# Kernel tuning notes

Hardware: AMD Instinct MI355X
Metric: run time of the kernel (lower is better)

## Reference

```python
import jax, jax.numpy as jnp
import numpy as np

B, T, D, H, O = 64, 2048, 64, 512, 128


def setup_inputs() -> dict:
    key = jax.random.key(0)
    ks = jax.random.split(key, 7)
    s = 1.0 / np.sqrt(H).astype(np.float32)  # PyTorch default uniform(-1/sqrt(H), 1/sqrt(H))
    u = lambda k, shp: jax.random.uniform(k, shp, jnp.float32, -s, s)
    return {
        "x": jax.random.normal(ks[0], (B, T, D), jnp.float32),
        "W_ih": u(ks[1], (4 * H, D)),
        "W_hh": u(ks[2], (4 * H, H)),
        "b_ih": u(ks[3], (4 * H,)),
        "b_hh": u(ks[4], (4 * H,)),
        "W_out": u(ks[5], (O, H)),
        "b_out": u(ks[6], (O,)),
        "batch_size": B,
    }


def reference(x, W_ih, W_hh, b_ih, b_hh, W_out, b_out, batch_size):
    Bv, Tv, Dv = x.shape
    Hv = W_hh.shape[1]
    # Precompute input-to-gate projections for all timesteps: [T, B, 4H]
    xg = (jnp.einsum("btd,gd->btg", x, W_ih) + b_ih + b_hh).transpose(1, 0, 2)
    h0 = jnp.zeros((Bv, Hv), x.dtype)
    c0 = jnp.zeros((Bv, Hv), x.dtype)

    def step(carry, g_t):
        h, c = carry
        g = g_t + h @ W_hh.T  # [B, 4H]
        i, f, gc, o = jnp.split(g, 4, axis=-1)  # PyTorch gate order i,f,g,o
        i = jax.nn.sigmoid(i)
        f = jax.nn.sigmoid(f)
        gc = jnp.tanh(gc)
        o = jax.nn.sigmoid(o)
        c = f * c + i * gc
        h = o * jnp.tanh(c)
        return (h, c), None

    (hT, cT), _ = jax.lax.scan(step, (h0, c0), xg)
    # Linear applied at last timestep only (module returns predictions[:, -1, :])
    pred = hT @ W_out.T + b_out  # [B, O]
    return pred, hT[None], cT[None]  # (pred, h_n[1,B,H], c_n[1,B,H])
```

## Files before the change

kernel.cpp:

```cpp
#include <hip/hip_runtime.h>
#include <hip/hip_bf16.h>


typedef short short8 __attribute__((ext_vector_type(8)));
typedef float floatx4 __attribute__((ext_vector_type(4)));

#define T_STEPS 2048
#define NBG 4
#define NGI 32
#define SB() __builtin_amdgcn_sched_barrier(0)

__device__ __forceinline__ unsigned short f2bf(float f){
    unsigned u = __builtin_bit_cast(unsigned, f);
    u += 0x7FFFu + ((u >> 16) & 1u);
    return (unsigned short)(u >> 16);
}

__device__ __forceinline__ short8 pack8(float4 a, float4 b){
    short8 s;
    s[0]=(short)f2bf(a.x); s[1]=(short)f2bf(a.y); s[2]=(short)f2bf(a.z); s[3]=(short)f2bf(a.w);
    s[4]=(short)f2bf(b.x); s[5]=(short)f2bf(b.y); s[6]=(short)f2bf(b.z); s[7]=(short)f2bf(b.w);
    return s;
}

__device__ __forceinline__ float fsigmoid(float x){ return 1.0f/(1.0f+__expf(-x)); }
__device__ __forceinline__ float ftanh(float x){ return 2.0f*fsigmoid(2.0f*x)-1.0f; }

__device__ __forceinline__ void xload4(float4* X, const float* base){
    asm volatile(
    "global_load_dwordx4 %0, %4, off\n\t"
    "global_load_dwordx4 %1, %4, off offset:16\n\t"
    "global_load_dwordx4 %2, %4, off offset:128\n\t"
    "global_load_dwordx4 %3, %4, off offset:144"
    : "=&v"(X[0]), "=&v"(X[1]), "=&v"(X[2]), "=&v"(X[3])
    : "v"(base) : "memory");
}

__device__ __forceinline__ void hload16_sc1(short8* A, const unsigned short* base){
    asm volatile(
    "global_load_dwordx4 %0, %16, off sc1\n\t"
    "global_load_dwordx4 %1, %16, off offset:64 sc1\n\t"
    "global_load_dwordx4 %2, %16, off offset:128 sc1\n\t"
    "global_load_dwordx4 %3, %16, off offset:192 sc1\n\t"
    "global_load_dwordx4 %4, %16, off offset:256 sc1\n\t"
    "global_load_dwordx4 %5, %16, off offset:320 sc1\n\t"
    "global_load_dwordx4 %6, %16, off offset:384 sc1\n\t"
    "global_load_dwordx4 %7, %16, off offset:448 sc1\n\t"
    "global_load_dwordx4 %8, %16, off offset:512 sc1\n\t"
    "global_load_dwordx4 %9, %16, off offset:576 sc1\n\t"
    "global_load_dwordx4 %10, %16, off offset:640 sc1\n\t"
    "global_load_dwordx4 %11, %16, off offset:704 sc1\n\t"
    "global_load_dwordx4 %12, %16, off offset:768 sc1\n\t"
    "global_load_dwordx4 %13, %16, off offset:832 sc1\n\t"
    "global_load_dwordx4 %14, %16, off offset:896 sc1\n\t"
    "global_load_dwordx4 %15, %16, off offset:960 sc1"
    : "=&v"(A[0]), "=&v"(A[1]), "=&v"(A[2]), "=&v"(A[3]),
      "=&v"(A[4]), "=&v"(A[5]), "=&v"(A[6]), "=&v"(A[7]),
      "=&v"(A[8]), "=&v"(A[9]), "=&v"(A[10]), "=&v"(A[11]),
      "=&v"(A[12]), "=&v"(A[13]), "=&v"(A[14]), "=&v"(A[15])
    : "v"(base) : "memory");
}

__global__ __launch_bounds__(64, 1)
void lstm_persist(const float* __restrict__ x,
                  const float* __restrict__ W_ih,
                  const float* __restrict__ W_hh,
                  const float* __restrict__ b_ih,
                  const float* __restrict__ b_hh,
                  const float* __restrict__ W_out,
                  const float* __restrict__ b_out,
                  float* __restrict__ out,
                  unsigned short* __restrict__ hbuf,
                  unsigned* __restrict__ flags)
{
    const int wg   = blockIdx.x;
    const int bg   = wg & 3;
    const int gi   = wg >> 2;
    const int lane = threadIdx.x;
    const int ln   = lane & 15;
    const int lk   = lane >> 4;
    const int hd0  = gi << 4;

    __shared__ __align__(16) unsigned short hl[256];

    short8 bw[4][18];
#pragma unroll
    for (int g = 0; g < 4; ++g){
        const int row = g * 512 + hd0 + ln;
        const float* pih = W_ih + row * 64 + lk * 8;
#pragma unroll
        for (int kk = 0; kk < 2; ++kk){
            float4 u0 = *reinterpret_cast<const float4*>(pih + kk * 32);
            float4 u1 = *reinterpret_cast<const float4*>(pih + kk * 32 + 4);
            bw[g][kk] = pack8(u0, u1);
        }
        const float* phh = W_hh + row * 512 + lk * 8;
#pragma unroll
        for (int kk = 2; kk < 18; ++kk){
            float4 u0 = *reinterpret_cast<const float4*>(phh + (kk - 2) * 32);
            float4 u1 = *reinterpret_cast<const float4*>(phh + (kk - 2) * 32 + 4);
            bw[g][kk] = pack8(u0, u1);
        }
    }

    float bias[4];
#pragma unroll
    for (int g = 0; g < 4; ++g){
        const int col = g * 512 + hd0 + ln;
        bias[g] = b_ih[col] + b_hh[col];
    }

    float c0 = 0.f, c1 = 0.f, c2 = 0.f, c3 = 0.f;
    const int xrow = bg * 16 + ln;

    const unsigned* fpoll = flags + bg * NGI + (lane & 31);
    unsigned* fme = flags + bg * NGI + gi;
    const unsigned one = 1u;

    short8 a[18];
    short8 stv = {0,0,0,0,0,0,0,0};
    float4 xr[4];
    xload4(xr, x + ((size_t)xrow * T_STEPS) * 64 + lk * 8);

    for (int t = 0; t < T_STEPS; ++t){
        const unsigned short* hp =
            hbuf + (size_t)((((t & 1) ^ 1) * NBG + bg) * 16 + ln) * 512 + lk * 8;

        if (t > 0){
            unsigned fv;
            do {
                asm volatile("global_load_dword %0, %1, off sc1\n\t"
                             "s_waitcnt vmcnt(0)"
                             : "=v"(fv) : "v"(fpoll) : "memory");
            } while (!__all((int)(fv >= (unsigned)t)));
            SB();
            asm volatile("" :: "v"(stv));
            hload16_sc1(&a[2], hp);
        } else {
            asm volatile("s_waitcnt vmcnt(0)" ::: "memory");
            SB();
            asm volatile("" :: "v"(stv));
        }

        a[0] = pack8(xr[0], xr[1]);
        a[1] = pack8(xr[2], xr[3]);

        floatx4 acc0 = {bias[0], bias[0], bias[0], bias[0]};
        floatx4 acc1 = {bias[1], bias[1], bias[1], bias[1]};
        floatx4 acc2 = {bias[2], bias[2], bias[2], bias[2]};
        floatx4 acc3 = {bias[3], bias[3], bias[3], bias[3]};
#pragma unroll
        for (int kk = 0; kk < 2; ++kk){
            acc0 = __builtin_amdgcn_mfma_f32_16x16x32_bf16(a[kk], bw[0][kk], acc0, 0, 0, 0);
            acc1 = __builtin_amdgcn_mfma_f32_16x16x32_bf16(a[kk], bw[1][kk], acc1, 0, 0, 0);
            acc2 = __builtin_amdgcn_mfma_f32_16x16x32_bf16(a[kk], bw[2][kk], acc2, 0, 0, 0);
            acc3 = __builtin_amdgcn_mfma_f32_16x16x32_bf16(a[kk], bw[3][kk], acc3, 0, 0, 0);
        }

        if (t > 0){
            asm volatile("s_waitcnt vmcnt(0)" ::: "memory");
            SB();
            const unsigned expst = (((unsigned)(t - 1) >> 1) & 1u) + 1u;
            for (;;){
                int ok = 1;
#pragma unroll
                for (int c = 2; c < 18; ++c){
                    unsigned s = ((unsigned)(unsigned short)a[c][6] & 1u)
                               | (((unsigned)(unsigned short)a[c][7] & 1u) << 1);
                    ok &= (s == expst) ? 1 : 0;
                }
                if (__all(ok)) break;
                hload16_sc1(&a[2], hp);
                asm volatile("s_waitcnt vmcnt(0)" ::: "memory");
                SB();
            }
#pragma unroll
            for (int kk = 2; kk < 18; ++kk){
                acc0 = __builtin_amdgcn_mfma_f32_16x16x32_bf16(a[kk], bw[0][kk], acc0, 0, 0, 0);
                acc1 = __builtin_amdgcn_mfma_f32_16x16x32_bf16(a[kk], bw[1][kk], acc1, 0, 0, 0);
                acc2 = __builtin_amdgcn_mfma_f32_16x16x32_bf16(a[kk], bw[2][kk], acc2, 0, 0, 0);
                acc3 = __builtin_amdgcn_mfma_f32_16x16x32_bf16(a[kk], bw[3][kk], acc3, 0, 0, 0);
            }
        }

#define EPI(R, CREG)                                                         \
        {   float iv = fsigmoid(acc0[R]);                                    \
            float fv_ = fsigmoid(acc1[R]);                                   \
            float gv = ftanh(acc2[R]);                                       \
            float ov = fsigmoid(acc3[R]);                                    \
            CREG = fv_ * CREG + iv * gv;                                     \
            float hv = ov * ftanh(CREG);                                     \
            hl[(lk * 4 + R) * 16 + ln] = f2bf(hv);                           \
            if (t == T_STEPS - 1){                                           \
                int rr = bg * 16 + lk * 4 + R;                               \
                out[8192  + rr * 512 + hd0 + ln] = hv;                       \
                out[40960 + rr * 512 + hd0 + ln] = CREG;                     \
            }                                                                \
        }
        EPI(0, c0) EPI(1, c1) EPI(2, c2) EPI(3, c3)
#undef EPI

        {
            const int tn = (t + 1 < T_STEPS) ? (t + 1) : t;
            xload4(xr, x + ((size_t)xrow * T_STEPS + (size_t)tn) * 64 + lk * 8);
        }

        asm volatile("s_waitcnt lgkmcnt(0)" ::: "memory");

        {
            const unsigned stamp = (((unsigned)t >> 1) & 1u) + 1u;
            if (lane < 32){
                const int row = lane >> 1, half = lane & 1;
                short8 v = *reinterpret_cast<const short8*>(&hl[row * 16 + half * 8]);
                v[6] = (short)((v[6] & ~(short)1) | (short)(stamp & 1u));
                v[7] = (short)((v[7] & ~(short)1) | (short)((stamp >> 1) & 1u));
                stv = v;
                unsigned short* dst =
                    hbuf + (size_t)(((t & 1) * NBG + bg) * 16 + row) * 512 + hd0 + half * 8;
                asm volatile("global_store_dwordx4 %0, %1, off sc1"
                             :: "v"(dst), "v"(stv) : "memory");
            }
            if (lane == 0){
                asm volatile("global_atomic_add %0, %1, off sc1"
                             :: "v"(fme), "v"(one) : "memory");
            }
        }
    }

    if (gi == 0){
        unsigned fv;
        do {
            asm volatile("global_load_dword %0, %1, off sc1\n\t"
                         "s_waitcnt vmcnt(0)"
                         : "=v"(fv) : "v"(fpoll) : "memory");
        } while (!__all((int)(fv >= (unsigned)T_STEPS)));
        SB();
        const unsigned expst = (((unsigned)(T_STEPS - 1) >> 1) & 1u) + 1u;
        const unsigned short* hp =
            hbuf + (size_t)((1 * NBG + bg) * 16 + ln) * 512 + lk * 8;
        short8 ha[16];
        int ok;
        do {
            hload16_sc1(ha, hp);
            asm volatile("s_waitcnt vmcnt(0)" ::: "memory");
            SB();
            ok = 1;
#pragma unroll
            for (int kk = 0; kk < 16; ++kk){
                unsigned s = ((unsigned)(unsigned short)ha[kk][6] & 1u)
                           | (((unsigned)(unsigned short)ha[kk][7] & 1u) << 1);
                ok &= (s == expst) ? 1 : 0;
            }
        } while (!__all(ok));
        SB();
#pragma unroll
        for (int o0 = 0; o0 < 8; ++o0){
            const int col = o0 * 16 + ln;
            const float* wp = W_out + col * 512 + lk * 8;
            floatx4 pa = {0.f, 0.f, 0.f, 0.f};
#pragma unroll
            for (int kk = 0; kk < 16; ++kk){
                float4 w0 = *reinterpret_cast<const float4*>(wp + kk * 32);
                float4 w1 = *reinterpret_cast<const float4*>(wp + kk * 32 + 4);
                pa = __builtin_amdgcn_mfma_f32_16x16x32_bf16(ha[kk], pack8(w0, w1), pa, 0, 0, 0);
            }
            const float bo = b_out[col];
#pragma unroll
            for (int r = 0; r < 4; ++r){
                const int rr = bg * 16 + lk * 4 + r;
                out[rr * 128 + col] = pa[r] + bo;
            }
        }
    }
}

extern "C" void kernel_launch(void* const* d_in, const int* in_sizes, int n_in,
                              void* d_out, int out_size, void* d_ws, size_t ws_size,
                              hipStream_t stream) {
    const float* x     = (const float*)d_in[0];
    const float* W_ih  = (const float*)d_in[1];
    const float* W_hh  = (const float*)d_in[2];
    const float* b_ih  = (const float*)d_in[3];
    const float* b_hh  = (const float*)d_in[4];
    const float* W_out = (const float*)d_in[5];
    const float* b_out = (const float*)d_in[6];

    const size_t HBUF_BYTES = (size_t)2 * NBG * 16 * 512 * 2;
    unsigned short* hbuf = (unsigned short*)d_ws;
    unsigned* flags = (unsigned*)((char*)d_ws + HBUF_BYTES);

    hipMemsetAsync(hbuf, 0, HBUF_BYTES, stream);
    hipMemsetAsync(flags, 0, NBG * NGI * sizeof(unsigned), stream);
    lstm_persist<<<dim3(NBG * NGI), dim3(64), 0, stream>>>(
        x, W_ih, W_hh, b_ih, b_hh, W_out, b_out,
        (float*)d_out, hbuf, flags);
}
```

Baseline: 6.783 ms.

## Spread workgroups across XCDs and rework cross-block handoff coherence

Launches 256 workgroups and maps them so that batch group is wg&7 with half the groups exiting early. With round-robin XCD dispatch, each batch group's blocks then land on one XCD, which may let a cheaper cache scope serve the exchange. The h-state loads switch from sc1 to sc0 scope, and polling alternates between sc0 and sc1. The store is now followed by a vmcnt wait before the flag atomic, replacing the stamp-bit validation loop at the end. This trades the stamp-based retry scheme for store-then-signal ordering, and relies on the co-location assumption for correctness.

```diff
diff --git a/kernel.cpp b/kernel.cpp
--- a/kernel.cpp
+++ b/kernel.cpp
@@ -33,6 +33,31 @@
     "global_load_dwordx4 %2, %4, off offset:128\n\t"
     "global_load_dwordx4 %3, %4, off offset:144"
     : "=&v"(X[0]), "=&v"(X[1]), "=&v"(X[2]), "=&v"(X[3])
+    : "v"(base) : "memory");
+}
+
+__device__ __forceinline__ void hload16_sc0(short8* A, const unsigned short* base){
+    asm volatile(
+    "global_load_dwordx4 %0, %16, off sc0\n\t"
+    "global_load_dwordx4 %1, %16, off offset:64 sc0\n\t"
+    "global_load_dwordx4 %2, %16, off offset:128 sc0\n\t"
+    "global_load_dwordx4 %3, %16, off offset:192 sc0\n\t"
+    "global_load_dwordx4 %4, %16, off offset:256 sc0\n\t"
+    "global_load_dwordx4 %5, %16, off offset:320 sc0\n\t"
+    "global_load_dwordx4 %6, %16, off offset:384 sc0\n\t"
+    "global_load_dwordx4 %7, %16, off offset:448 sc0\n\t"
+    "global_load_dwordx4 %8, %16, off offset:512 sc0\n\t"
+    "global_load_dwordx4 %9, %16, off offset:576 sc0\n\t"
+    "global_load_dwordx4 %10, %16, off offset:640 sc0\n\t"
+    "global_load_dwordx4 %11, %16, off offset:704 sc0\n\t"
+    "global_load_dwordx4 %12, %16, off offset:768 sc0\n\t"
+    "global_load_dwordx4 %13, %16, off offset:832 sc0\n\t"
+    "global_load_dwordx4 %14, %16, off offset:896 sc0\n\t"
+    "global_load_dwordx4 %15, %16, off offset:960 sc0"
+    : "=&v"(A[0]), "=&v"(A[1]), "=&v"(A[2]), "=&v"(A[3]),
+      "=&v"(A[4]), "=&v"(A[5]), "=&v"(A[6]), "=&v"(A[7]),
+      "=&v"(A[8]), "=&v"(A[9]), "=&v"(A[10]), "=&v"(A[11]),
+      "=&v"(A[12]), "=&v"(A[13]), "=&v"(A[14]), "=&v"(A[15])
     : "v"(base) : "memory");
 }
 
@@ -74,8 +99,9 @@
                   unsigned* __restrict__ flags)
 {
     const int wg   = blockIdx.x;
-    const int bg   = wg & 3;
-    const int gi   = wg >> 2;
+    const int bg   = wg & 7;
+    const int gi   = wg >> 3;
+    if (bg >= NBG) return;
     const int lane = threadIdx.x;
     const int ln   = lane & 15;
     const int lk   = lane >> 4;
@@ -118,7 +144,6 @@
     const unsigned one = 1u;
 
     short8 a[18];
-    short8 stv = {0,0,0,0,0,0,0,0};
     float4 xr[4];
     xload4(xr, x + ((size_t)xrow * T_STEPS) * 64 + lk * 8);
 
@@ -127,19 +152,25 @@
             hbuf + (size_t)((((t & 1) ^ 1) * NBG + bg) * 16 + ln) * 512 + lk * 8;
 
         if (t > 0){
-            unsigned fv;
-            do {
-                asm volatile("global_load_dword %0, %1, off sc1\n\t"
-                             "s_waitcnt vmcnt(0)"
-                             : "=v"(fv) : "v"(fpoll) : "memory");
-            } while (!__all((int)(fv >= (unsigned)t)));
+            unsigned fv; int sw = 0;
+            for (;;){
+                if (sw & 1){
+                    asm volatile("global_load_dword %0, %1, off sc1\n\t"
+                                 "s_waitcnt vmcnt(0)"
+                                 : "=v"(fv) : "v"(fpoll) : "memory");
+                } else {
+                    asm volatile("global_load_dword %0, %1, off sc0\n\t"
+                                 "s_waitcnt vmcnt(0)"
+                                 : "=v"(fv) : "v"(fpoll) : "memory");
+                }
+                ++sw;
+                if (__all((int)(fv >= (unsigned)t))) break;
+            }
             SB();
-            asm volatile("" :: "v"(stv));
-            hload16_sc1(&a[2], hp);
+            hload16_sc0(&a[2], hp);
         } else {
             asm volatile("s_waitcnt vmcnt(0)" ::: "memory");
             SB();
-            asm volatile("" :: "v"(stv));
         }
 
         a[0] = pack8(xr[0], xr[1]);
@@ -214,16 +245,17 @@
                 short8 v = *reinterpret_cast<const short8*>(&hl[row * 16 + half * 8]);
                 v[6] = (short)((v[6] & ~(short)1) | (short)(stamp & 1u));
                 v[7] = (short)((v[7] & ~(short)1) | (short)((stamp >> 1) & 1u));
-                stv = v;
                 unsigned short* dst =
                     hbuf + (size_t)(((t & 1) * NBG + bg) * 16 + row) * 512 + hd0 + half * 8;
                 asm volatile("global_store_dwordx4 %0, %1, off sc1"
-                             :: "v"(dst), "v"(stv) : "memory");
-            }
-            if (lane == 0){
-                asm volatile("global_atomic_add %0, %1, off sc1"
-                             :: "v"(fme), "v"(one) : "memory");
-            }
+                             :: "v"(dst), "v"(v) : "memory");
+            }
+        }
+        asm volatile("s_waitcnt vmcnt(0)" ::: "memory");
+        SB();
+        if (lane == 0){
+            asm volatile("global_atomic_add %0, %1, off sc1"
+                         :: "v"(fme), "v"(one) : "memory");
         }
     }
 
@@ -235,23 +267,11 @@
                          : "=v"(fv) : "v"(fpoll) : "memory");
         } while (!__all((int)(fv >= (unsigned)T_STEPS)));
         SB();
-        const unsigned expst = (((unsigned)(T_STEPS - 1) >> 1) & 1u) + 1u;
         const unsigned short* hp =
             hbuf + (size_t)((1 * NBG + bg) * 16 + ln) * 512 + lk * 8;
         short8 ha[16];
-        int ok;
-        do {
-            hload16_sc1(ha, hp);
-            asm volatile("s_waitcnt vmcnt(0)" ::: "memory");
-            SB();
-            ok = 1;
-#pragma unroll
-            for (int kk = 0; kk < 16; ++kk){
-                unsigned s = ((unsigned)(unsigned short)ha[kk][6] & 1u)
-                           | (((unsigned)(unsigned short)ha[kk][7] & 1u) << 1);
-                ok &= (s == expst) ? 1 : 0;
-            }
-        } while (!__all(ok));
+        hload16_sc1(ha, hp);
+        asm volatile("s_waitcnt vmcnt(0)" ::: "memory");
         SB();
 #pragma unroll
         for (int o0 = 0; o0 < 8; ++o0){
@@ -291,7 +311,7 @@
 
     hipMemsetAsync(hbuf, 0, HBUF_BYTES, stream);
     hipMemsetAsync(flags, 0, NBG * NGI * sizeof(unsigned), stream);
-    lstm_persist<<<dim3(NBG * NGI), dim3(64), 0, stream>>>(
+    lstm_persist<<<dim3(256), dim3(64), 0, stream>>>(
         x, W_ih, W_hh, b_ih, b_hh, W_out, b_out,
         (float*)d_out, hbuf, flags);
 }
```

Measured after the change: 7.609 ms. 1.12x slower.
